# Kernel optimization log

Hardware: AMD Instinct MI355X
Metric: run time of the kernel (lower is better)

The kernel has to match this reference:

```python
import jax, jax.numpy as jnp
import numpy as np

B, T, IN, HID, G = 64, 500, 1024, 1024, 8
IG = IN // G   # per-group input size = 128
HG = HID // G  # per-group hidden size = 128


def setup_inputs() -> dict:
    key = jax.random.key(0)
    k0, k1, k2, k3, k4 = jax.random.split(key, 5)
    s = 1.0 / np.sqrt(HG)  # torch GRU init: U(-1/sqrt(hidden), 1/sqrt(hidden))
    x = jax.random.normal(k0, (B, T, IN), dtype=jnp.float32)
    W_ih = jax.random.uniform(k1, (G, 3 * HG, IG), jnp.float32, -s, s)  # gate order r,z,n
    W_hh = jax.random.uniform(k2, (G, 3 * HG, HG), jnp.float32, -s, s)
    b_ih = jax.random.uniform(k3, (G, 3 * HG), jnp.float32, -s, s)
    b_hh = jax.random.uniform(k4, (G, 3 * HG), jnp.float32, -s, s)
    return {"x": x, "W_ih": W_ih, "W_hh": W_hh, "b_ih": b_ih, "b_hh": b_hh}


def reference(x, W_ih, W_hh, b_ih, b_hh):
    b, t, _ = x.shape
    g, h3, ig = W_ih.shape
    hg = h3 // 3
    xg = x.reshape(b, t, g, ig)  # split channels into groups
    # precompute input projections for all timesteps/groups: [B,T,G,3*HG]
    xp = jnp.einsum('btgi,gji->btgj', xg, W_ih) + b_ih
    h0 = jnp.zeros((b, g, hg), x.dtype)

    def step(h, xt):
        # h: [B,G,HG], xt: [B,G,3*HG]
        hp = jnp.einsum('bgh,gjh->bgj', h, W_hh) + b_hh
        xr, xz, xn = jnp.split(xt, 3, axis=-1)
        hr, hz, hn = jnp.split(hp, 3, axis=-1)
        r = jax.nn.sigmoid(xr + hr)
        z = jax.nn.sigmoid(xz + hz)
        n = jnp.tanh(xn + r * hn)
        h_new = (1.0 - z) * n + z * h
        return h_new, h_new

    _, hs = jax.lax.scan(step, h0, jnp.moveaxis(xp, 1, 0))  # hs: [T,B,G,HG]
    out = jnp.moveaxis(hs, 0, 1).reshape(b, t, g * hg)  # concat groups on last dim
    return out
```

## Files before the change

### kernel.cpp

```cpp
#include <hip/hip_runtime.h>
#include <math.h>

#define B_   64
#define T_   500
#define IN_  1024
#define G_   8
#define HG_  128
#define J3_  384

typedef _Float16 half8 __attribute__((ext_vector_type(8)));
typedef _Float16 half4 __attribute__((ext_vector_type(4)));
typedef float    f32x4 __attribute__((ext_vector_type(4)));

#define S_RZ (-1.44269504f)
#define S_N  (-2.88539008f)

static __device__ __forceinline__ half8 cvt_half8_s(const float* p, float s) {
    const float4 a = *(const float4*)p;
    const float4 b = *(const float4*)(p + 4);
    half8 h;
    h[0]=(_Float16)(a.x*s); h[1]=(_Float16)(a.y*s); h[2]=(_Float16)(a.z*s); h[3]=(_Float16)(a.w*s);
    h[4]=(_Float16)(b.x*s); h[5]=(_Float16)(b.y*s); h[6]=(_Float16)(b.z*s); h[7]=(_Float16)(b.w*s);
    return h;
}

static __device__ __forceinline__ void pin_frag(half8& h) {
    f32x4 t = __builtin_bit_cast(f32x4, h);
    float a = t[0], b = t[1], c = t[2], d = t[3];
    asm volatile("" : "+v"(a), "+v"(b), "+v"(c), "+v"(d));
    t[0] = a; t[1] = b; t[2] = c; t[3] = d;
    h = __builtin_bit_cast(half8, t);
}
static __device__ __forceinline__ void pin_f32x4(f32x4& v) {
    float a = v[0], b = v[1], c = v[2], d = v[3];
    asm volatile("" : "+v"(a), "+v"(b), "+v"(c), "+v"(d));
    v[0] = a; v[1] = b; v[2] = c; v[3] = d;
}

static __device__ __forceinline__ void barrier_lds_only() {
    asm volatile("s_waitcnt lgkmcnt(0)\n\ts_barrier" ::: "memory");
}

static __device__ __forceinline__ float sel4(f32x4 v, int rsel) {
    const float t0 = (rsel & 1) ? v[1] : v[0];
    const float t1 = (rsel & 1) ? v[3] : v[2];
    return (rsel & 2) ? t1 : t0;
}

#define MFMA16(A,Bv,C) __builtin_amdgcn_mfma_f32_16x16x32_f16((A),(Bv),(C),0,0,0)

__global__ __launch_bounds__(256)
void cvt_x(const float* __restrict__ x, _Float16* __restrict__ x16)
{
    const size_t n4 = (size_t)B_ * T_ * IN_ / 4;
    const size_t stride = (size_t)gridDim.x * 256;
    for (size_t i = (size_t)blockIdx.x * 256 + threadIdx.x; i < n4; i += stride) {
        const float4 v = ((const float4*)x)[i];
        half4 h;
        h[0] = (_Float16)v.x; h[1] = (_Float16)v.y;
        h[2] = (_Float16)v.z; h[3] = (_Float16)v.w;
        ((half4*)x16)[i] = h;
    }
}

__global__ __launch_bounds__(512, 1)
void gru_fused(const float* __restrict__ Wih, const float* __restrict__ Whh,
               const float* __restrict__ bih, const float* __restrict__ bhh,
               const _Float16* __restrict__ x16, float* __restrict__ out)
{
    const int tid  = threadIdx.x;
    const int lane = tid & 63;
    const int w    = tid >> 6;
    const int lr   = lane & 15;
    const int hi   = lane >> 4;
    const int blk  = blockIdx.x;
    const int g    = blk & 7;
    const int bp   = blk >> 3;
    const int sq   = lr & 1;
    const int rsel = (lr >> 1) & 3;
    const int jl   = w * 16 + hi * 4;
    const int jown = jl + rsel;
    const int bown = bp * 2 + sq;

    __shared__ _Float16 h16[2][2][HG_];
    __shared__ float    xmem[2][16][392];

    half8 aI[3][4], aH[3][4];
#pragma unroll
    for (int p = 0; p < 3; ++p)
#pragma unroll
        for (int kt = 0; kt < 4; ++kt) {
            const size_t roff = (size_t)(g * J3_ + p * 128 + w * 16 + lr) * HG_
                              + kt * 32 + hi * 8;
            const float s = (p == 2) ? S_N : S_RZ;
            aI[p][kt] = cvt_half8_s(Wih + roff, s);  pin_frag(aI[p][kt]);
            aH[p][kt] = cvt_half8_s(Whh + roff, s);  pin_frag(aH[p][kt]);
        }

    const float* bi = bih + g * J3_;
    const float* bh = bhh + g * J3_;
    f32x4 s0 = (*(const f32x4*)(bi + jl)       + *(const f32x4*)(bh + jl))       * S_RZ;
    f32x4 s1 = (*(const f32x4*)(bi + 128 + jl) + *(const f32x4*)(bh + 128 + jl)) * S_RZ;
    f32x4 s2 = (*(const f32x4*)(bi + 256 + jl)) * S_N;
    f32x4 bhn_s = (*(const f32x4*)(bh + 256 + jl)) * S_N;
    pin_f32x4(s0); pin_f32x4(s1); pin_f32x4(s2); pin_f32x4(bhn_s);

    float hreg = 0.f;
    if (tid < 256) h16[0][tid >> 7][tid & 127] = (_Float16)0.f;

    const _Float16* xcol = x16 + (size_t)(bp * 2 + (lr & 1)) * T_ * IN_ + g * HG_;
    float*          oown = out + (size_t)bown * T_ * IN_ + g * HG_ + jown;

    half8 bx[4];
    {
        const _Float16* px = xcol + (size_t)(lr >> 1) * IN_;
#pragma unroll
        for (int kt = 0; kt < 4; ++kt) bx[kt] = *(const half8*)(px + kt * 32 + hi * 8);
    }
    {
        f32x4 d0 = s0, d1 = s1, d2 = s2;
#pragma unroll
        for (int kt = 0; kt < 4; ++kt) {
            d0 = MFMA16(aI[0][kt], bx[kt], d0);
            d1 = MFMA16(aI[1][kt], bx[kt], d1);
            d2 = MFMA16(aI[2][kt], bx[kt], d2);
        }
        *(f32x4*)&xmem[0][lr][      w * 16 + hi * 4] = d0;
        *(f32x4*)&xmem[0][lr][128 + w * 16 + hi * 4] = d1;
        *(f32x4*)&xmem[0][lr][256 + w * 16 + hi * 4] = d2;
    }
    {
        int tn = 8 + (lr >> 1); if (tn > T_ - 1) tn = T_ - 1;
        const _Float16* px = xcol + (size_t)tn * IN_;
#pragma unroll
        for (int kt = 0; kt < 4; ++kt) bx[kt] = *(const half8*)(px + kt * 32 + hi * 8);
    }
    f32x4 pxa0, pxa1, pxa2;
    {
        const int xc = sq;
        pxa0 = *(const f32x4*)&xmem[0][xc][      jl];
        pxa1 = *(const f32x4*)&xmem[0][xc][128 + jl];
        pxa2 = *(const f32x4*)&xmem[0][xc][256 + jl];
    }
    f32x4 d0, d1, d2;

    __syncthreads();

#define REC_STEP(S)                                                                \
    do {                                                                           \
        const int pb = (S) & 1;                                                    \
                                                \
        const _Float16* hsrc = &h16[pb][sq][0];                                    \
        const half8 bf0 = *(const half8*)(hsrc +  0 + hi * 8);                     \
        const half8 bf1 = *(const half8*)(hsrc + 32 + hi * 8);                     \
        const half8 bf2 = *(const half8*)(hsrc + 64 + hi * 8);                     \
        const half8 bf3 = *(const half8*)(hsrc + 96 + hi * 8);                     \
               \
                  \
        if ((S) == 0) { d0 = s0; d1 = s1; d2 = s2; }                               \
        if ((S) < 4) {                                                             \
            d0 = MFMA16(aI[0][(S) & 3], bx[(S) & 3], d0);                          \
            d1 = MFMA16(aI[1][(S) & 3], bx[(S) & 3], d1);                          \
            d2 = MFMA16(aI[2][(S) & 3], bx[(S) & 3], d2);                          \
        }                                                                          \
                      \
        f32x4 h0 = pxa0, h1 = pxa1, h2 = bhn_s;                                    \
        h0 = MFMA16(aH[0][0], bf0, h0);                                            \
        h1 = MFMA16(aH[1][0], bf0, h1);                                            \
        h2 = MFMA16(aH[2][0], bf0, h2);                                            \
        h0 = MFMA16(aH[0][1], bf1, h0);                                            \
        h1 = MFMA16(aH[1][1], bf1, h1);                                            \
        h2 = MFMA16(aH[2][1], bf1, h2);                                            \
        h0 = MFMA16(aH[0][2], bf2, h0);                                            \
        h1 = MFMA16(aH[1][2], bf2, h1);                                            \
        h2 = MFMA16(aH[2][2], bf2, h2);                                            \
        h0 = MFMA16(aH[0][3], bf3, h0);                                            \
        h1 = MFMA16(aH[1][3], bf3, h1);                                            \
        h2 = MFMA16(aH[2][3], bf3, h2);                                            \
                    \
        if ((S) == 3) {                                                            \
            *(f32x4*)&xmem[xb ^ 1][lr][      w * 16 + hi * 4] = d0;                \
            *(f32x4*)&xmem[xb ^ 1][lr][128 + w * 16 + hi * 4] = d1;                \
            *(f32x4*)&xmem[xb ^ 1][lr][256 + w * 16 + hi * 4] = d2;                \
            int tn = t0 + 16 + (lr >> 1); if (tn > T_ - 1) tn = T_ - 1;            \
            const _Float16* px = xcol + (size_t)tn * IN_;                          \
            bx[0] = *(const half8*)(px +  0 + hi * 8);                             \
            bx[1] = *(const half8*)(px + 32 + hi * 8);                             \
            bx[2] = *(const half8*)(px + 64 + hi * 8);                             \
            bx[3] = *(const half8*)(px + 96 + hi * 8);                             \
        }                                                                          \
                            \
        {                                                                          \
            const int nxb = ((S) == 7) ? (xb ^ 1) : xb;                            \
            const int nxc = (((S) + 1) & 7) * 2 + sq;                              \
            pxa0 = *(const f32x4*)&xmem[nxb][nxc][      jl];                       \
            pxa1 = *(const f32x4*)&xmem[nxb][nxc][128 + jl];                       \
            pxa2 = *(const f32x4*)&xmem[nxb][nxc][256 + jl];                       \
        }                                                                          \
                        \
        const float ar = sel4(h0, rsel);                                           \
        const float az = sel4(h1, rsel);                                           \
        const float an = sel4(h2, rsel);                                           \
        const float xn = xn_cur;                                                   \
        const float rg = __builtin_amdgcn_rcpf(1.f + __builtin_amdgcn_exp2f(ar));  \
        const float zg = __builtin_amdgcn_rcpf(1.f + __builtin_amdgcn_exp2f(az));  \
        const float pre = xn + rg * an;                                            \
        const float th  = __builtin_fmaf(2.f,                                      \
            __builtin_amdgcn_rcpf(1.f + __builtin_amdgcn_exp2f(pre)), -1.f);       \
        const float hnew = __builtin_fmaf(zg, hreg - th, th);                      \
        hreg = hnew;                                                               \
                                \
        if (lr < 8) {                                                              \
            h16[pb ^ 1][sq][jown] = (_Float16)hnew;                                \
            oown[(size_t)(t0 + (S)) * IN_] = hnew;                                 \
        }                                                                          \
        barrier_lds_only();                                                        \
    } while (0)

    for (int t0 = 0; t0 < T_; t0 += 8) {
        const int xb = (t0 >> 3) & 1;
        {
            float xn_cur = sel4(pxa2, rsel);
            REC_STEP(0);
        }
        { float xn_cur = sel4(pxa2, rsel); REC_STEP(1); }
        { float xn_cur = sel4(pxa2, rsel); REC_STEP(2); }
        { float xn_cur = sel4(pxa2, rsel); REC_STEP(3); }
        if (t0 + 4 < T_) {
            { float xn_cur = sel4(pxa2, rsel); REC_STEP(4); }
            { float xn_cur = sel4(pxa2, rsel); REC_STEP(5); }
            { float xn_cur = sel4(pxa2, rsel); REC_STEP(6); }
            { float xn_cur = sel4(pxa2, rsel); REC_STEP(7); }
        }
    }
#undef REC_STEP
}

extern "C" void kernel_launch(void* const* d_in, const int* in_sizes, int n_in,
                              void* d_out, int out_size, void* d_ws, size_t ws_size,
                              hipStream_t stream) {
    (void)in_sizes; (void)n_in; (void)out_size; (void)ws_size;
    const float* x   = (const float*)d_in[0];
    const float* Wih = (const float*)d_in[1];
    const float* Whh = (const float*)d_in[2];
    const float* bih = (const float*)d_in[3];
    const float* bhh = (const float*)d_in[4];
    float* out = (float*)d_out;

    _Float16* x16 = (_Float16*)d_ws;

    cvt_x<<<4096, 256, 0, stream>>>(x, x16);
    gru_fused<<<256, 512, 0, stream>>>(Wih, Whh, bih, bhh, x16, out);
}
```

Before: 260.1 us.

## Map one batch per block and double grid with two blocks per CU

Each block now handles a single batch element per group instead of two, so the grid doubles to 512 blocks. The occupancy hint changes to four waves per EU so that two blocks can share a CU. The input-projection MFMA now covers 16 timesteps of one batch, and the recurrence loop unrolls 16 steps per chunk. The aim is to hide the latency of the serial recurrence by interleaving two independent blocks. In exchange, each recurrent MFMA uses only one useful column, and the tighter register budget may cause spills of the pinned weight fragments.

```diff
diff --git a/kernel.cpp b/kernel.cpp
--- a/kernel.cpp
+++ b/kernel.cpp
@@ -63,7 +63,7 @@
     }
 }
 
-__global__ __launch_bounds__(512, 1)
+__global__ __launch_bounds__(512) __attribute__((amdgpu_waves_per_eu(4, 4)))
 void gru_fused(const float* __restrict__ Wih, const float* __restrict__ Whh,
                const float* __restrict__ bih, const float* __restrict__ bhh,
                const _Float16* __restrict__ x16, float* __restrict__ out)
@@ -75,14 +75,12 @@
     const int hi   = lane >> 4;
     const int blk  = blockIdx.x;
     const int g    = blk & 7;
-    const int bp   = blk >> 3;
-    const int sq   = lr & 1;
-    const int rsel = (lr >> 1) & 3;
+    const int b    = blk >> 3;
+    const int rsel = lr & 3;
     const int jl   = w * 16 + hi * 4;
     const int jown = jl + rsel;
-    const int bown = bp * 2 + sq;
-
-    __shared__ _Float16 h16[2][2][HG_];
+
+    __shared__ _Float16 h16[2][HG_];
     __shared__ float    xmem[2][16][392];
 
     half8 aI[3][4], aH[3][4];
@@ -106,14 +104,14 @@
     pin_f32x4(s0); pin_f32x4(s1); pin_f32x4(s2); pin_f32x4(bhn_s);
 
     float hreg = 0.f;
-    if (tid < 256) h16[0][tid >> 7][tid & 127] = (_Float16)0.f;
-
-    const _Float16* xcol = x16 + (size_t)(bp * 2 + (lr & 1)) * T_ * IN_ + g * HG_;
-    float*          oown = out + (size_t)bown * T_ * IN_ + g * HG_ + jown;
+    if (tid < HG_) h16[0][tid] = (_Float16)0.f;
+
+    const _Float16* xcol = x16 + (size_t)b * T_ * IN_ + g * HG_;
+    float*          oown = out + (size_t)b * T_ * IN_ + g * HG_ + jown;
 
     half8 bx[4];
     {
-        const _Float16* px = xcol + (size_t)(lr >> 1) * IN_;
+        const _Float16* px = xcol + (size_t)lr * IN_;
 #pragma unroll
         for (int kt = 0; kt < 4; ++kt) bx[kt] = *(const half8*)(px + kt * 32 + hi * 8);
     }
@@ -130,18 +128,15 @@
         *(f32x4*)&xmem[0][lr][256 + w * 16 + hi * 4] = d2;
     }
     {
-        int tn = 8 + (lr >> 1); if (tn > T_ - 1) tn = T_ - 1;
+        int tn = 16 + lr; if (tn > T_ - 1) tn = T_ - 1;
         const _Float16* px = xcol + (size_t)tn * IN_;
 #pragma unroll
         for (int kt = 0; kt < 4; ++kt) bx[kt] = *(const half8*)(px + kt * 32 + hi * 8);
     }
     f32x4 pxa0, pxa1, pxa2;
-    {
-        const int xc = sq;
-        pxa0 = *(const f32x4*)&xmem[0][xc][      jl];
-        pxa1 = *(const f32x4*)&xmem[0][xc][128 + jl];
-        pxa2 = *(const f32x4*)&xmem[0][xc][256 + jl];
-    }
+    pxa0 = *(const f32x4*)&xmem[0][0][      jl];
+    pxa1 = *(const f32x4*)&xmem[0][0][128 + jl];
+    pxa2 = *(const f32x4*)&xmem[0][0][256 + jl];
     f32x4 d0, d1, d2;
 
     __syncthreads();
@@ -149,14 +144,13 @@
 #define REC_STEP(S)                                                                \
     do {                                                                           \
         const int pb = (S) & 1;                                                    \
-                                                \
-        const _Float16* hsrc = &h16[pb][sq][0];                                    \
+               \
+        const _Float16* hsrc = &h16[pb][0];                                        \
         const half8 bf0 = *(const half8*)(hsrc +  0 + hi * 8);                     \
         const half8 bf1 = *(const half8*)(hsrc + 32 + hi * 8);                     \
         const half8 bf2 = *(const half8*)(hsrc + 64 + hi * 8);                     \
         const half8 bf3 = *(const half8*)(hsrc + 96 + hi * 8);                     \
-               \
-                  \
+                          \
         if ((S) == 0) { d0 = s0; d1 = s1; d2 = s2; }                               \
         if ((S) < 4) {                                                             \
             d0 = MFMA16(aI[0][(S) & 3], bx[(S) & 3], d0);                          \
@@ -182,22 +176,22 @@
             *(f32x4*)&xmem[xb ^ 1][lr][      w * 16 + hi * 4] = d0;                \
             *(f32x4*)&xmem[xb ^ 1][lr][128 + w * 16 + hi * 4] = d1;                \
             *(f32x4*)&xmem[xb ^ 1][lr][256 + w * 16 + hi * 4] = d2;                \
-            int tn = t0 + 16 + (lr >> 1); if (tn > T_ - 1) tn = T_ - 1;            \
+            int tn = t0 + 32 + lr; if (tn > T_ - 1) tn = T_ - 1;                   \
             const _Float16* px = xcol + (size_t)tn * IN_;                          \
             bx[0] = *(const half8*)(px +  0 + hi * 8);                             \
             bx[1] = *(const half8*)(px + 32 + hi * 8);                             \
             bx[2] = *(const half8*)(px + 64 + hi * 8);                             \
             bx[3] = *(const half8*)(px + 96 + hi * 8);                             \
         }                                                                          \
-                            \
+                              \
         {                                                                          \
-            const int nxb = ((S) == 7) ? (xb ^ 1) : xb;                            \
-            const int nxc = (((S) + 1) & 7) * 2 + sq;                              \
+            const int nxb = ((S) == 15) ? (xb ^ 1) : xb;                           \
+            const int nxc = ((S) + 1) & 15;                                        \
             pxa0 = *(const f32x4*)&xmem[nxb][nxc][      jl];                       \
             pxa1 = *(const f32x4*)&xmem[nxb][nxc][128 + jl];                       \
             pxa2 = *(const f32x4*)&xmem[nxb][nxc][256 + jl];                       \
         }                                                                          \
-                        \
+                               \
         const float ar = sel4(h0, rsel);                                           \
         const float az = sel4(h1, rsel);                                           \
         const float an = sel4(h2, rsel);                                           \
@@ -209,28 +203,33 @@
             __builtin_amdgcn_rcpf(1.f + __builtin_amdgcn_exp2f(pre)), -1.f);       \
         const float hnew = __builtin_fmaf(zg, hreg - th, th);                      \
         hreg = hnew;                                                               \
-                                \
-        if (lr < 8) {                                                              \
-            h16[pb ^ 1][sq][jown] = (_Float16)hnew;                                \
+                              \
+        if (lr < 4) {                                                              \
+            h16[pb ^ 1][jown] = (_Float16)hnew;                                    \
             oown[(size_t)(t0 + (S)) * IN_] = hnew;                                 \
         }                                                                          \
         barrier_lds_only();                                                        \
     } while (0)
 
-    for (int t0 = 0; t0 < T_; t0 += 8) {
-        const int xb = (t0 >> 3) & 1;
-        {
-            float xn_cur = sel4(pxa2, rsel);
-            REC_STEP(0);
-        }
-        { float xn_cur = sel4(pxa2, rsel); REC_STEP(1); }
-        { float xn_cur = sel4(pxa2, rsel); REC_STEP(2); }
-        { float xn_cur = sel4(pxa2, rsel); REC_STEP(3); }
+    for (int t0 = 0; t0 < T_; t0 += 16) {
+        const int xb = (t0 >> 4) & 1;
+        { float xn_cur = sel4(pxa2, rsel); REC_STEP(0);  }
+        { float xn_cur = sel4(pxa2, rsel); REC_STEP(1);  }
+        { float xn_cur = sel4(pxa2, rsel); REC_STEP(2);  }
+        { float xn_cur = sel4(pxa2, rsel); REC_STEP(3);  }
         if (t0 + 4 < T_) {
-            { float xn_cur = sel4(pxa2, rsel); REC_STEP(4); }
-            { float xn_cur = sel4(pxa2, rsel); REC_STEP(5); }
-            { float xn_cur = sel4(pxa2, rsel); REC_STEP(6); }
-            { float xn_cur = sel4(pxa2, rsel); REC_STEP(7); }
+            { float xn_cur = sel4(pxa2, rsel); REC_STEP(4);  }
+            { float xn_cur = sel4(pxa2, rsel); REC_STEP(5);  }
+            { float xn_cur = sel4(pxa2, rsel); REC_STEP(6);  }
+            { float xn_cur = sel4(pxa2, rsel); REC_STEP(7);  }
+            { float xn_cur = sel4(pxa2, rsel); REC_STEP(8);  }
+            { float xn_cur = sel4(pxa2, rsel); REC_STEP(9);  }
+            { float xn_cur = sel4(pxa2, rsel); REC_STEP(10); }
+            { float xn_cur = sel4(pxa2, rsel); REC_STEP(11); }
+            { float xn_cur = sel4(pxa2, rsel); REC_STEP(12); }
+            { float xn_cur = sel4(pxa2, rsel); REC_STEP(13); }
+            { float xn_cur = sel4(pxa2, rsel); REC_STEP(14); }
+            { float xn_cur = sel4(pxa2, rsel); REC_STEP(15); }
         }
     }
 #undef REC_STEP
@@ -250,5 +249,5 @@
     _Float16* x16 = (_Float16*)d_ws;
 
     cvt_x<<<4096, 256, 0, stream>>>(x, x16);
-    gru_fused<<<256, 512, 0, stream>>>(Wih, Whh, bih, bhh, x16, out);
-}
+    gru_fused<<<512, 512, 0, stream>>>(Wih, Whh, bih, bhh, x16, out);
+}
```

New measurement: 503.0 us. 1.93x slower.
